# Kernel optimization log

Hardware: AMD Instinct MI355X
Metric: run time of the kernel (lower is better)

The kernel has to match this reference:

```python
import jax, jax.numpy as jnp
import numpy as np

M_PER_GROUP = 16
EPS = 0.001


def setup_inputs() -> dict:
    key = jax.random.key(0)
    x = jax.random.normal(key, (32, 64, 64, 256), dtype=jnp.float32)
    return {"x": x}


def reference(x) -> jnp.ndarray:
    # x: [B, W, H, C] (NHWC). Training-phase path, decomposition='cholesky', renorm=False.
    b, w, h, c = x.shape
    groups = c // M_PER_GROUP
    n = b * w * h  # samples per channel

    # [C, B*W*H]
    x_flat = jnp.transpose(x, (3, 0, 1, 2)).reshape(c, -1)
    mean = jnp.mean(x_flat, axis=1, keepdims=True)          # [C, 1]
    f = x_flat - mean                                        # [C, N]

    # per-group covariance: [G, m, N] -> [G, m, m]
    fg = f.reshape(groups, M_PER_GROUP, -1)
    denom = jnp.float32(n) - 1.0
    cov = jnp.einsum('gmn,gkn->gmk', fg, fg) / denom
    eye = jnp.eye(M_PER_GROUP, dtype=x.dtype)
    cov = (1.0 - EPS) * cov + EPS * eye
    # NOTE: the original TF code divides by (N-1) a second time after shrinkage;
    # reproduced faithfully here.
    cov = cov / denom

    # batched Cholesky + triangular solve: inv_sqrt = L^{-1}
    chol = jnp.linalg.cholesky(cov)                          # [G, m, m], lower
    inv_sqrt = jax.vmap(
        lambda L: jax.scipy.linalg.solve_triangular(L, eye, lower=True)
    )(chol)                                                  # [G, m, m]

    # whiten: [G, m, m] @ [G, m, N] -> [G, m, N]
    f_hat = jnp.einsum('gmk,gkn->gmn', inv_sqrt, fg)
    out = f_hat.reshape(c, b, w, h)
    return jnp.transpose(out, (1, 2, 3, 0))
```

## Files before the change

kernel.cpp:

```cpp
#include <hip/hip_runtime.h>


#define NROWS   131072
#define DENOMF  131071.0f
#define EPSV    0.001f

#define OFF_INV    0
#define OFF_BIAS   4096
#define OFF_RED    4352
#define OFF_PART   151808
#define GS2        9216

typedef __attribute__((ext_vector_type(8))) short bf16x8;
typedef __attribute__((ext_vector_type(4))) float f32x4;
typedef __attribute__((ext_vector_type(4))) unsigned int u32x4;

__device__ __forceinline__ unsigned int fbits(float v) {
    return __builtin_bit_cast(unsigned int, v);
}
__device__ __forceinline__ float bfloat(unsigned int u) {
    return __builtin_bit_cast(float, u);
}

struct Row8 { float a, b, c, d, e, f, g, h; };

__device__ __forceinline__ void cvt8(const Row8 r, bf16x8& hv, bf16x8& lv, float& s) {
    s += ((r.a + r.b) + (r.c + r.d)) + ((r.e + r.f) + (r.g + r.h));
    const unsigned int ua = fbits(r.a), ub = fbits(r.b), uc = fbits(r.c), ud = fbits(r.d);
    const unsigned int ue = fbits(r.e), uf = fbits(r.f), ug = fbits(r.g), uh = fbits(r.h);
    u32x4 hp;
    hp.x = (ub & 0xFFFF0000u) | (ua >> 16);
    hp.y = (ud & 0xFFFF0000u) | (uc >> 16);
    hp.z = (uf & 0xFFFF0000u) | (ue >> 16);
    hp.w = (uh & 0xFFFF0000u) | (ug >> 16);
    const float da = r.a - bfloat(ua & 0xFFFF0000u);
    const float db = r.b - bfloat(ub & 0xFFFF0000u);
    const float dc = r.c - bfloat(uc & 0xFFFF0000u);
    const float dd = r.d - bfloat(ud & 0xFFFF0000u);
    const float de = r.e - bfloat(ue & 0xFFFF0000u);
    const float df = r.f - bfloat(uf & 0xFFFF0000u);
    const float dg = r.g - bfloat(ug & 0xFFFF0000u);
    const float dh = r.h - bfloat(uh & 0xFFFF0000u);
    u32x4 lp;
    lp.x = (fbits(db) & 0xFFFF0000u) | (fbits(da) >> 16);
    lp.y = (fbits(dd) & 0xFFFF0000u) | (fbits(dc) >> 16);
    lp.z = (fbits(df) & 0xFFFF0000u) | (fbits(de) >> 16);
    lp.w = (fbits(dh) & 0xFFFF0000u) | (fbits(dg) >> 16);
    hv = __builtin_bit_cast(bf16x8, hp);
    lv = __builtin_bit_cast(bf16x8, lp);
}

__global__ __launch_bounds__(512, 4) void k1_stats(const float* __restrict__ x,
                                                   float* __restrict__ ws, int NB) {
    __shared__ float xt[64 * 260];
    const int tid = threadIdx.x;
    const int lane = tid & 63, wv = tid >> 6;
    const int slot = lane >> 4;
    const int TPB = (NROWS / 64) / NB;
    const float4* gf4 = reinterpret_cast<const float4*>(x);
    const size_t tile0 = (size_t)blockIdx.x * TPB;

    const int g0 = wv * 2;
    const int rb0 = g0 * 16 + (lane & 15);
    const int roA0 = (slot * 8 + ((0 + 2 * slot) & 7)) * 260 + rb0;
    const int roA1 = (slot * 8 + ((1 + 2 * slot) & 7)) * 260 + rb0;
    const int roA2 = (slot * 8 + ((2 + 2 * slot) & 7)) * 260 + rb0;
    const int roA3 = (slot * 8 + ((3 + 2 * slot) & 7)) * 260 + rb0;
    const int roA4 = (slot * 8 + ((4 + 2 * slot) & 7)) * 260 + rb0;
    const int roA5 = (slot * 8 + ((5 + 2 * slot) & 7)) * 260 + rb0;
    const int roA6 = (slot * 8 + ((6 + 2 * slot) & 7)) * 260 + rb0;
    const int roA7 = (slot * 8 + ((7 + 2 * slot) & 7)) * 260 + rb0;
    const int roB0 = roA0 + 32 * 260, roB1 = roA1 + 32 * 260;
    const int roB2 = roA2 + 32 * 260, roB3 = roA3 + 32 * 260;
    const int roB4 = roA4 + 32 * 260, roB5 = roA5 + 32 * 260;
    const int roB6 = roA6 + 32 * 260, roB7 = roA7 + 32 * 260;

    f32x4 hh0 = {0,0,0,0}, hl0 = {0,0,0,0}, ll0 = {0,0,0,0};
    f32x4 hh1 = {0,0,0,0}, hl1 = {0,0,0,0}, ll1 = {0,0,0,0};
    float s0 = 0.f, s1 = 0.f;

    float4 st0, st1, st2, st3, st4, st5, st6, st7;
#define LOADT(T)                                                              \
    {                                                                         \
        const float4* tp = gf4 + (tile0 + (T)) * 4096 + tid;                  \
        st0 = tp[0];    st1 = tp[512];  st2 = tp[1024]; st3 = tp[1536];       \
        st4 = tp[2048]; st5 = tp[2560]; st6 = tp[3072]; st7 = tp[3584];       \
    }
#define WRK(K, ST)                                                            \
    {                                                                         \
        const int idx = tid + (K) * 512;                                      \
        *reinterpret_cast<float4*>(&xt[(idx >> 6) * 260 + (idx & 63) * 4]) = ST; \
    }
#define PROCG(U, G, AHH, AHL, ALL, S)                                         \
    {                                                                         \
        Row8 r;                                                               \
        r.a = xt[ro##U##0 + (G) * 16]; r.b = xt[ro##U##1 + (G) * 16];         \
        r.c = xt[ro##U##2 + (G) * 16]; r.d = xt[ro##U##3 + (G) * 16];         \
        r.e = xt[ro##U##4 + (G) * 16]; r.f = xt[ro##U##5 + (G) * 16];         \
        r.g = xt[ro##U##6 + (G) * 16]; r.h = xt[ro##U##7 + (G) * 16];         \
        bf16x8 hv, lv;                                                        \
        cvt8(r, hv, lv, S);                                                   \
        AHH = __builtin_amdgcn_mfma_f32_16x16x32_bf16(hv, hv, AHH, 0, 0, 0);  \
        AHL = __builtin_amdgcn_mfma_f32_16x16x32_bf16(hv, lv, AHL, 0, 0, 0);  \
        ALL = __builtin_amdgcn_mfma_f32_16x16x32_bf16(lv, lv, ALL, 0, 0, 0);  \
    }

    LOADT(0);
    for (int t = 0; t < TPB; ++t) {
        __syncthreads();
        WRK(0, st0); WRK(1, st1); WRK(2, st2); WRK(3, st3);
        WRK(4, st4); WRK(5, st5); WRK(6, st6); WRK(7, st7);
        __syncthreads();
        const int tn = (t + 1 < TPB) ? (t + 1) : t;
        LOADT(tn);
        PROCG(A, 0, hh0, hl0, ll0, s0);
        PROCG(B, 0, hh0, hl0, ll0, s0);
        PROCG(A, 1, hh1, hl1, ll1, s1);
        PROCG(B, 1, hh1, hl1, ll1, s1);
    }
#undef PROCG
#undef WRK
#undef LOADT

    float* pb = ws + OFF_PART + (size_t)blockIdx.x * GS2 + (size_t)g0 * 576;
#define STG(G, AHH, AHL, ALL, S)                                              \
    {                                                                         \
        float* pw = pb + (G) * 576;                                           \
        pw[0 * 64 + lane] = AHH[0] + ALL[0];                                  \
        pw[1 * 64 + lane] = AHH[1] + ALL[1];                                  \
        pw[2 * 64 + lane] = AHH[2] + ALL[2];                                  \
        pw[3 * 64 + lane] = AHH[3] + ALL[3];                                  \
        pw[4 * 64 + lane] = AHL[0]; pw[5 * 64 + lane] = AHL[1];               \
        pw[6 * 64 + lane] = AHL[2]; pw[7 * 64 + lane] = AHL[3];               \
        pw[8 * 64 + lane] = S;                                                \
    }
    STG(0, hh0, hl0, ll0, s0);
    STG(1, hh1, hl1, ll1, s1);
#undef STG
}

__global__ __launch_bounds__(256, 4) void k2_reduce(float* __restrict__ ws, int NB) {
    const int t = blockIdx.x * 256 + threadIdx.x;
    if (t >= GS2) return;
    const int per = NB / 16;
    const float* p = ws + OFF_PART + (size_t)(blockIdx.y * per) * GS2 + t;
    float sum = 0.f;
#pragma unroll 8
    for (int b = 0; b < per; ++b) sum += p[(size_t)b * GS2];
    ws[OFF_RED + (size_t)blockIdx.y * GS2 + t] = sum;
}

__device__ __forceinline__ void chol_from_sg(const float* sg, int g, int tid,
                                             float* __restrict__ ws) {
    const int ii = tid & 15;
    const float inv_denom = 1.0f / DENOMF;
    const float cs_ii = sg[512 + ii] + sg[512 + 16 + ii] +
                        sg[512 + 32 + ii] + sg[512 + 48 + ii];
    const float mu_l = cs_ii * (1.0f / (float)NROWS);

#define GIDX2(T, I, J) ((T) * 256 + ((I) & 3) * 64 + ((((I) >> 2)) << 4) + (J))
    float arow[16];
#pragma unroll
    for (int kk = 0; kk < 16; ++kk) {
        float G = sg[GIDX2(0, ii, kk)] + sg[GIDX2(1, ii, kk)] + sg[GIDX2(1, kk, ii)];
        float mu_k = __shfl(mu_l, kk, 64);
        float cv = (G - (float)NROWS * mu_l * mu_k) * inv_denom;
        cv = cv * (1.0f - EPSV) + ((kk == ii) ? EPSV : 0.0f);
        arow[kk] = cv * inv_denom;
    }
#undef GIDX2

    float lrow[16];
#pragma unroll
    for (int j = 0; j < 16; ++j) {
        float diag = __shfl(arow[j], j, 64);
        float ljj  = sqrtf(diag);
        float lij  = (ii == j) ? ljj : arow[j] / ljj;
        lrow[j] = lij;
#pragma unroll
        for (int k = j + 1; k < 16; ++k) {
            float lkj = __shfl(lij, k, 64);
            arow[k] = fmaf(-lij, lkj, arow[k]);
        }
    }

    float xcol[16];
#pragma unroll
    for (int i2 = 0; i2 < 16; ++i2) {
        float ssum = (ii == i2) ? 1.0f : 0.0f;
#pragma unroll
        for (int k = 0; k < 16; ++k) {
            if (k < i2) {
                float Lik = __shfl(lrow[k], i2, 64);
                ssum = fmaf(-Lik, xcol[k], ssum);
            }
        }
        float Lii = __shfl(lrow[i2], i2, 64);
        xcol[i2] = (i2 >= ii) ? ssum / Lii : 0.0f;
    }

    float* invg = ws + OFF_INV + g * 256;
#pragma unroll
    for (int i2 = 0; i2 < 16; ++i2) {
        if (tid < 16) invg[i2 * 16 + tid] = xcol[i2];
        float bi = xcol[i2] * mu_l;
        bi += __shfl_xor(bi, 1, 64);
        bi += __shfl_xor(bi, 2, 64);
        bi += __shfl_xor(bi, 4, 64);
        bi += __shfl_xor(bi, 8, 64);
        if (tid == 0) ws[OFF_BIAS + g * 16 + i2] = bi;
    }
}

__global__ void k2_chol(float* __restrict__ ws, int NB) {
    __shared__ float sg[576];
    const int g = blockIdx.x, tid = threadIdx.x;

    for (int e = tid; e < 576; e += 64) {
        float v = 0.f;
#pragma unroll
        for (int y = 0; y < 16; ++y)
            v += ws[OFF_RED + (size_t)y * GS2 + g * 576 + e];
        sg[e] = v;
    }
    __syncthreads();
    chol_from_sg(sg, g, tid, ws);
}

template <int CTRL>
__device__ __forceinline__ float dpp1(float v) {
    int iv = __builtin_bit_cast(int, v);
    int r = __builtin_amdgcn_update_dpp(iv, iv, CTRL, 0xF, 0xF, false);
    return __builtin_bit_cast(float, r);
}
template <int CTRL>
__device__ __forceinline__ float4 dpp4(float4 v) {
    float4 r;
    r.x = dpp1<CTRL>(v.x);
    r.y = dpp1<CTRL>(v.y);
    r.z = dpp1<CTRL>(v.z);
    r.w = dpp1<CTRL>(v.w);
    return r;
}

#define DOT4(O, A, V) \
    O = fmaf(A.x, V.x, O); O = fmaf(A.y, V.y, O); \
    O = fmaf(A.z, V.z, O); O = fmaf(A.w, V.w, O)

__global__ __launch_bounds__(256, 4) void k3_apply(const float* __restrict__ x,
                                                   const float* __restrict__ ws,
                                                   float* __restrict__ out) {
    const int tid = threadIdx.x, lane = tid & 63, wv = tid >> 6;
    const int q = lane & 3, g = lane >> 2;

    const float* invg = ws + OFF_INV + g * 256;
#define LOADIR(R, M) \
    *reinterpret_cast<const float4*>(invg + (4 * q + (R)) * 16 + 4 * (q ^ (M)))
    float4 ir00 = LOADIR(0, 0), ir01 = LOADIR(0, 1), ir02 = LOADIR(0, 2), ir03 = LOADIR(0, 3);
    float4 ir10 = LOADIR(1, 0), ir11 = LOADIR(1, 1), ir12 = LOADIR(1, 2), ir13 = LOADIR(1, 3);
    float4 ir20 = LOADIR(2, 0), ir21 = LOADIR(2, 1), ir22 = LOADIR(2, 2), ir23 = LOADIR(2, 3);
    float4 ir30 = LOADIR(3, 0), ir31 = LOADIR(3, 1), ir32 = LOADIR(3, 2), ir33 = LOADIR(3, 3);
#undef LOADIR
    float4 b4 = *reinterpret_cast<const float4*>(ws + OFF_BIAS + g * 16 + 4 * q);

    const int rpb   = NROWS / gridDim.x;
    const int iters = rpb / 4;
    const size_t rowbase = (size_t)blockIdx.x * rpb;
    const float4* xp = reinterpret_cast<const float4*>(x) + rowbase * 64 + lane;
    float4*       op = reinterpret_cast<float4*>(out)     + rowbase * 64 + lane;

    float4 cur = xp[(size_t)wv * 64];
    for (int i = 0; i < iters; ++i) {
        const int ip = (i + 1 < iters) ? (i + 1) : (iters - 1);
        float4 nxt = xp[(size_t)(ip * 4 + wv) * 64];

        float4 v0 = cur;
        float4 v1 = dpp4<0xB1>(cur);
        float4 v2 = dpp4<0x4E>(cur);
        float4 v3 = dpp4<0x1B>(cur);

        float o0 = -b4.x, o1 = -b4.y, o2 = -b4.z, o3 = -b4.w;
        DOT4(o0, ir00, v0); DOT4(o0, ir01, v1); DOT4(o0, ir02, v2); DOT4(o0, ir03, v3);
        DOT4(o1, ir10, v0); DOT4(o1, ir11, v1); DOT4(o1, ir12, v2); DOT4(o1, ir13, v3);
        DOT4(o2, ir20, v0); DOT4(o2, ir21, v1); DOT4(o2, ir22, v2); DOT4(o2, ir23, v3);
        DOT4(o3, ir30, v0); DOT4(o3, ir31, v1); DOT4(o3, ir32, v2); DOT4(o3, ir33, v3);

        op[(size_t)(i * 4 + wv) * 64] = make_float4(o0, o1, o2, o3);
        cur = nxt;
    }
}

extern "C" void kernel_launch(void* const* d_in, const int* in_sizes, int n_in,
                              void* d_out, int out_size, void* d_ws, size_t ws_size,
                              hipStream_t stream) {
    const float* x = (const float*)d_in[0];
    float* out = (float*)d_out;
    float* ws  = (float*)d_ws;

    int NB = 128;
    if (ws_size >= (size_t)(OFF_PART + 512 * GS2) * sizeof(float)) NB = 512;
    else if (ws_size >= (size_t)(OFF_PART + 256 * GS2) * sizeof(float)) NB = 256;

    k1_stats<<<NB, 512, 0, stream>>>(x, ws, NB);
    dim3 rg((GS2 + 255) / 256, 16);
    k2_reduce<<<rg, 256, 0, stream>>>(ws, NB);
    k2_chol<<<16, 64, 0, stream>>>(ws, NB);
    k3_apply<<<1024, 256, 0, stream>>>(x, ws, out);
}
```

Baseline: 97.13 us.

## Double-buffer stats tiles in LDS with direct global-to-LDS async loads

The statistics kernel now streams each 64-row tile straight from global memory into LDS using global_load_lds (16-byte) instead of going through registers and explicit LDS stores. It double-buffers the LDS tile so the next tile's load is in flight while the current one feeds the MFMA covariance accumulation, and it drops one barrier per iteration. LDS use doubles, so occupancy is lowered to 2 blocks in the launch bounds, and the block count is capped at 256. The larger LDS footprint may allow only one block per CU and could reduce latency hiding.

New measurement: 89.80 us. 1.08x faster.

```diff
diff --git a/kernel.cpp b/kernel.cpp
--- a/kernel.cpp
+++ b/kernel.cpp
@@ -20,6 +20,12 @@
 }
 __device__ __forceinline__ float bfloat(unsigned int u) {
     return __builtin_bit_cast(float, u);
+}
+
+__device__ __forceinline__ void gload_lds16(float* lds, const float* g) {
+    __builtin_amdgcn_global_load_lds(
+        (const __attribute__((address_space(1))) unsigned int*)g,
+        (__attribute__((address_space(3))) unsigned int*)lds, 16, 0, 0);
 }
 
 struct Row8 { float a, b, c, d, e, f, g, h; };
@@ -50,14 +56,13 @@
     lv = __builtin_bit_cast(bf16x8, lp);
 }
 
-__global__ __launch_bounds__(512, 4) void k1_stats(const float* __restrict__ x,
+__global__ __launch_bounds__(512, 2) void k1_stats(const float* __restrict__ x,
                                                    float* __restrict__ ws, int NB) {
-    __shared__ float xt[64 * 260];
+    __shared__ float xt[2][64 * 260];
     const int tid = threadIdx.x;
     const int lane = tid & 63, wv = tid >> 6;
     const int slot = lane >> 4;
     const int TPB = (NROWS / 64) / NB;
-    const float4* gf4 = reinterpret_cast<const float4*>(x);
     const size_t tile0 = (size_t)blockIdx.x * TPB;
 
     const int g0 = wv * 2;
@@ -79,48 +84,51 @@
     f32x4 hh1 = {0,0,0,0}, hl1 = {0,0,0,0}, ll1 = {0,0,0,0};
     float s0 = 0.f, s1 = 0.f;
 
-    float4 st0, st1, st2, st3, st4, st5, st6, st7;
-#define LOADT(T)                                                              \
+#define STAGE(B, T)                                                           \
     {                                                                         \
-        const float4* tp = gf4 + (tile0 + (T)) * 4096 + tid;                  \
-        st0 = tp[0];    st1 = tp[512];  st2 = tp[1024]; st3 = tp[1536];       \
-        st4 = tp[2048]; st5 = tp[2560]; st6 = tp[3072]; st7 = tp[3584];       \
-    }
-#define WRK(K, ST)                                                            \
+        const float* gp = x + ((tile0 + (T)) * 64 + (size_t)(wv * 8)) * 256   \
+                            + (size_t)lane * 4;                               \
+        float* lb = &xt[B][(wv * 8) * 260];                                   \
+        gload_lds16(lb + 0 * 260, gp + 0 * 256);                              \
+        gload_lds16(lb + 1 * 260, gp + 1 * 256);                              \
+        gload_lds16(lb + 2 * 260, gp + 2 * 256);                              \
+        gload_lds16(lb + 3 * 260, gp + 3 * 256);                              \
+        gload_lds16(lb + 4 * 260, gp + 4 * 256);                              \
+        gload_lds16(lb + 5 * 260, gp + 5 * 256);                              \
+        gload_lds16(lb + 6 * 260, gp + 6 * 256);                              \
+        gload_lds16(lb + 7 * 260, gp + 7 * 256);                              \
+    }
+#define PROCG(BUF, U, G, AHH, AHL, ALL, S)                                    \
     {                                                                         \
-        const int idx = tid + (K) * 512;                                      \
-        *reinterpret_cast<float4*>(&xt[(idx >> 6) * 260 + (idx & 63) * 4]) = ST; \
-    }
-#define PROCG(U, G, AHH, AHL, ALL, S)                                         \
-    {                                                                         \
+        const float* bp = &xt[BUF][0];                                        \
         Row8 r;                                                               \
-        r.a = xt[ro##U##0 + (G) * 16]; r.b = xt[ro##U##1 + (G) * 16];         \
-        r.c = xt[ro##U##2 + (G) * 16]; r.d = xt[ro##U##3 + (G) * 16];         \
-        r.e = xt[ro##U##4 + (G) * 16]; r.f = xt[ro##U##5 + (G) * 16];         \
-        r.g = xt[ro##U##6 + (G) * 16]; r.h = xt[ro##U##7 + (G) * 16];         \
+        r.a = bp[ro##U##0 + (G) * 16]; r.b = bp[ro##U##1 + (G) * 16];         \
+        r.c = bp[ro##U##2 + (G) * 16]; r.d = bp[ro##U##3 + (G) * 16];         \
+        r.e = bp[ro##U##4 + (G) * 16]; r.f = bp[ro##U##5 + (G) * 16];         \
+        r.g = bp[ro##U##6 + (G) * 16]; r.h = bp[ro##U##7 + (G) * 16];         \
         bf16x8 hv, lv;                                                        \
         cvt8(r, hv, lv, S);                                                   \
         AHH = __builtin_amdgcn_mfma_f32_16x16x32_bf16(hv, hv, AHH, 0, 0, 0);  \
         AHL = __builtin_amdgcn_mfma_f32_16x16x32_bf16(hv, lv, AHL, 0, 0, 0);  \
         ALL = __builtin_amdgcn_mfma_f32_16x16x32_bf16(lv, lv, ALL, 0, 0, 0);  \
     }
-
-    LOADT(0);
-    for (int t = 0; t < TPB; ++t) {
+#define PROC4(BUF)                                                            \
+    PROCG(BUF, A, 0, hh0, hl0, ll0, s0);                                      \
+    PROCG(BUF, B, 0, hh0, hl0, ll0, s0);                                      \
+    PROCG(BUF, A, 1, hh1, hl1, ll1, s1);                                      \
+    PROCG(BUF, B, 1, hh1, hl1, ll1, s1);
+
+    STAGE(0, 0);
+    for (int t = 0; t < TPB - 1; ++t) {
         __syncthreads();
-        WRK(0, st0); WRK(1, st1); WRK(2, st2); WRK(3, st3);
-        WRK(4, st4); WRK(5, st5); WRK(6, st6); WRK(7, st7);
-        __syncthreads();
-        const int tn = (t + 1 < TPB) ? (t + 1) : t;
-        LOADT(tn);
-        PROCG(A, 0, hh0, hl0, ll0, s0);
-        PROCG(B, 0, hh0, hl0, ll0, s0);
-        PROCG(A, 1, hh1, hl1, ll1, s1);
-        PROCG(B, 1, hh1, hl1, ll1, s1);
-    }
+        STAGE((t + 1) & 1, t + 1);
+        PROC4(t & 1);
+    }
+    __syncthreads();
+    PROC4((TPB - 1) & 1);
+#undef PROC4
 #undef PROCG
-#undef WRK
-#undef LOADT
+#undef STAGE
 
     float* pb = ws + OFF_PART + (size_t)blockIdx.x * GS2 + (size_t)g0 * 576;
 #define STG(G, AHH, AHL, ALL, S)                                              \
@@ -298,8 +306,7 @@
     float* ws  = (float*)d_ws;
 
     int NB = 128;
-    if (ws_size >= (size_t)(OFF_PART + 512 * GS2) * sizeof(float)) NB = 512;
-    else if (ws_size >= (size_t)(OFF_PART + 256 * GS2) * sizeof(float)) NB = 256;
+    if (ws_size >= (size_t)(OFF_PART + 256 * GS2) * sizeof(float)) NB = 256;
 
     k1_stats<<<NB, 512, 0, stream>>>(x, ws, NB);
     dim3 rg((GS2 + 255) / 256, 16);
```
